# Kernel tuning notes

Measured on AMD Instinct MI355X. Metric: run time of the kernel, lower is better.

The kernel has to match this reference:

```python
import jax, jax.numpy as jnp
import numpy as np

B, S, DIM = 2, 2048, 4096
H, KV = 32, 8
HD = DIM // H          # 128
REP = H // KV          # 4


def _rope_tables(seq_len, head_dim, base=10000.0):
    inv_freq = 1.0 / (base ** (jnp.arange(0, head_dim, 2, dtype=jnp.float32) / head_dim))
    t = jnp.arange(seq_len, dtype=jnp.float32)
    freqs = jnp.outer(t, inv_freq)                      # [S, D/2]
    emb = jnp.concatenate([freqs, freqs], axis=-1)      # [S, D]
    return jnp.cos(emb)[:, None, :], jnp.sin(emb)[:, None, :]  # [S,1,D]


def setup_inputs() -> dict:
    key = jax.random.key(0)
    kx, kq, kk, kv, ko = jax.random.split(key, 5)
    x = jax.random.normal(kx, (B, S, DIM), dtype=jnp.float32)
    cos, sin = _rope_tables(S, HD)
    s = 0.02
    Wq = jax.random.normal(kq, (DIM, H * HD), dtype=jnp.float32) * s
    Wk = jax.random.normal(kk, (DIM, KV * HD), dtype=jnp.float32) * s
    Wv = jax.random.normal(kv, (DIM, KV * HD), dtype=jnp.float32) * s
    Wo = jax.random.normal(ko, (H * HD, DIM), dtype=jnp.float32) * s
    return {"x": x, "cos": cos, "sin": sin, "Wq": Wq, "Wk": Wk, "Wv": Wv, "Wo": Wo}


def _rotate_half(t):
    t1, t2 = jnp.split(t, 2, axis=-1)
    return jnp.concatenate([-t2, t1], axis=-1)


def reference(x, cos, sin, Wq, Wk, Wv, Wo):
    b, s, _ = x.shape
    q = (x @ Wq).reshape(b, s, H, HD)
    k = (x @ Wk).reshape(b, s, KV, HD)
    v = (x @ Wv).reshape(b, s, KV, HD)
    # RoPE (cos/sin broadcast [S,1,D] -> [B,S,H,D])
    q = q * cos + _rotate_half(q) * sin
    k = k * cos + _rotate_half(k) * sin
    # grouped-head attention: avoid materializing repeated K/V
    q = q.reshape(b, s, KV, REP, HD)
    scale = 1.0 / jnp.sqrt(jnp.asarray(HD, dtype=x.dtype))
    scores = jnp.einsum('bqgrd,bkgd->bgrqk', q, k) * scale  # [B,KV,REP,S,S]
    causal = jnp.tril(jnp.ones((s, s), dtype=bool))
    scores = jnp.where(causal, scores, jnp.finfo(scores.dtype).min)
    attn = jax.nn.softmax(scores, axis=-1)
    out = jnp.einsum('bgrqk,bkgd->bqgrd', attn, v)          # [B,S,KV,REP,HD]
    out = out.reshape(b, s, H * HD)
    return out @ Wo
```

## Files before the change

### kernel.cpp

```cpp
#include <hip/hip_runtime.h>
#include <hip/hip_bf16.h>

#define B_   2
#define S_   2048
#define DIM_ 4096
#define H_   32
#define KV_  8
#define HD_  128
#define MROWS_ (B_ * S_)
#define KVD_ (KV_ * HD_)
#define QKVN_ (DIM_ + 2 * KVD_)

typedef __attribute__((ext_vector_type(8))) short short8;
typedef __attribute__((ext_vector_type(4))) float floatx4;

__device__ __forceinline__ unsigned int f2bf(float f) {
    union { float f; unsigned int u; } v; v.f = f;
    unsigned int lsb = (v.u >> 16) & 1u;
    v.u += 0x7fffu + lsb;
    return v.u >> 16;
}
__device__ __forceinline__ unsigned int pack2bf(float lo, float hi) {
    return f2bf(lo) | (f2bf(hi) << 16);
}

__device__ __forceinline__ uint4 load8cvt(const float* __restrict__ src) {
    const float4 a = ((const float4*)src)[0];
    const float4 b = ((const float4*)src)[1];
    uint4 r;
    r.x = pack2bf(a.x, a.y);
    r.y = pack2bf(a.z, a.w);
    r.z = pack2bf(b.x, b.y);
    r.w = pack2bf(b.z, b.w);
    return r;
}

__device__ __forceinline__ void storeC(float* p, float v) { *p = v; }
__device__ __forceinline__ void storeC(__hip_bfloat16* p, float v) { *p = __float2bfloat16(v); }

__device__ __forceinline__ void gload16(const unsigned short* g, unsigned short* l)
{
    __builtin_amdgcn_global_load_lds(
        (const __attribute__((address_space(1))) void*)g,
        (__attribute__((address_space(3))) void*)l,
        16, 0, 0);
}

__global__ __launch_bounds__(256)
void convert_bf16(const float* __restrict__ X, unsigned short* __restrict__ Y, int total8)
{
    const int i = blockIdx.x * 256 + threadIdx.x;
    if (i >= total8) return;
    uint4 v = load8cvt(X + (size_t)i * 8);
    *(uint4*)(Y + (size_t)i * 8) = v;
}

__global__ __launch_bounds__(256)
void wtrans(const float* __restrict__ W, unsigned short* __restrict__ Wt, int K, int N)
{
    __shared__ float tile[64][65];
    const int n0 = blockIdx.x * 64;
    const int k0 = blockIdx.y * 64;
    const int t  = threadIdx.x;
    #pragma unroll
    for (int it = 0; it < 4; ++it) {
        const int seg = t + it * 256;
        const int r   = seg >> 4;
        const int c   = (seg & 15) << 2;
        const float4 v = *(const float4*)&W[(size_t)(k0 + r) * N + n0 + c];
        tile[r][c]     = v.x;
        tile[r][c + 1] = v.y;
        tile[r][c + 2] = v.z;
        tile[r][c + 3] = v.w;
    }
    __syncthreads();
    const int n  = t >> 2;
    const int ks = (t & 3) << 4;
    unsigned int ob[8];
    #pragma unroll
    for (int j = 0; j < 8; ++j)
        ob[j] = pack2bf(tile[ks + 2 * j][n], tile[ks + 2 * j + 1][n]);
    uint4* dst = (uint4*)&Wt[(size_t)(n0 + n) * K + k0 + ks];
    dst[0] = ((const uint4*)ob)[0];
    dst[1] = ((const uint4*)ob)[1];
}

template <typename TC>
__global__ __launch_bounds__(256)
void gemm_bt(const unsigned short* __restrict__ A,
             const unsigned short* __restrict__ Bt,
             TC* __restrict__ C,
             int M, int N, int K)
{
    __shared__ unsigned short As[128 * 32];
    __shared__ unsigned short Bs[128 * 32];

    const int tid  = threadIdx.x;
    const int lane = tid & 63;
    const int w    = tid >> 6;
    const int wm   = (w >> 1) * 64;
    const int wn   = (w & 1) * 64;

    const int gx  = gridDim.x;
    const int nwg = gx * gridDim.y;
    int lid = blockIdx.y * gx + blockIdx.x;
    if ((nwg & 7) == 0) {
        const int q = nwg >> 3;
        lid = (lid & 7) * q + (lid >> 3);
    }
    const int m0 = (lid / gx) * 128;
    const int n0 = (lid % gx) * 128;

    const int fm   = lane & 15;
    const int fk   = (lane >> 4) * 8;

    floatx4 acc[4][4] = {};

    const int sr = tid >> 2;
    const int sk = (tid & 3) * 8;
    const unsigned short* ga0 = A  + (size_t)(m0 + sr) * K + sk;
    const unsigned short* ga1 = ga0 + (size_t)64 * K;
    const unsigned short* gb0 = Bt + (size_t)(n0 + sr) * K + sk;
    const unsigned short* gb1 = gb0 + (size_t)64 * K;
    unsigned short* lA = As + w * 512;
    unsigned short* lB = Bs + w * 512;

    for (int k0 = 0; k0 < K; k0 += 32) {
        gload16(ga0 + k0, lA);
        gload16(ga1 + k0, lA + 2048);
        gload16(gb0 + k0, lB);
        gload16(gb1 + k0, lB + 2048);
        __syncthreads();

        short8 af[4], bf[4];
        #pragma unroll
        for (int i = 0; i < 4; ++i) {
            af[i] = *(const short8*)&As[(wm + i * 16 + fm) * 32 + fk];
            bf[i] = *(const short8*)&Bs[(wn + i * 16 + fm) * 32 + fk];
        }
        #pragma unroll
        for (int mi = 0; mi < 4; ++mi)
            #pragma unroll
            for (int ni = 0; ni < 4; ++ni)
                acc[mi][ni] = __builtin_amdgcn_mfma_f32_16x16x32_bf16(
                    af[mi], bf[ni], acc[mi][ni], 0, 0, 0);
        __syncthreads();
    }

    const int cl = lane & 15;
    const int rq = (lane >> 4) * 4;
    #pragma unroll
    for (int mi = 0; mi < 4; ++mi) {
        #pragma unroll
        for (int ni = 0; ni < 4; ++ni) {
            const int col = n0 + wn + ni * 16 + cl;
            #pragma unroll
            for (int r = 0; r < 4; ++r) {
                const int row = m0 + wm + mi * 16 + rq + r;
                storeC(C + (size_t)row * N + col, acc[mi][ni][r]);
            }
        }
    }
}

__global__ void rope_kernel(unsigned short* __restrict__ T,
                            const float* __restrict__ cosb,
                            const float* __restrict__ sinb,
                            int NH, int coloff, int total)
{
    int idx = blockIdx.x * blockDim.x + threadIdx.x;
    if (idx >= total) return;
    const int dh   = idx & 63;
    const int rest = idx >> 6;
    const int h    = rest % NH;
    const int bs   = rest / NH;
    const int s    = bs & (S_ - 1);
    const size_t base = (size_t)bs * QKVN_ + coloff + h * HD_;
    const float t1 = __bfloat162float(*(__hip_bfloat16*)&T[base + dh]);
    const float t2 = __bfloat162float(*(__hip_bfloat16*)&T[base + dh + 64]);
    const float c1 = cosb[s * HD_ + dh];
    const float s1 = sinb[s * HD_ + dh];
    const float c2 = cosb[s * HD_ + dh + 64];
    const float s2 = sinb[s * HD_ + dh + 64];
    T[base + dh]      = (unsigned short)f2bf(t1 * c1 - t2 * s1);
    T[base + dh + 64] = (unsigned short)f2bf(t2 * c2 + t1 * s2);
}

__global__ __launch_bounds__(256)
void attn_mfma(const unsigned short* __restrict__ QKV,
               __hip_bfloat16* __restrict__ O)
{
    const int bx = blockIdx.x;
    const int bh = blockIdx.y;
    const int b  = bh >> 5;
    const int h  = bh & 31;
    const int g  = h >> 2;

    __shared__ unsigned short lds[27136];
    unsigned short* KsF = lds;
    unsigned short* VtF = lds + 8704;
    unsigned short* PsF = lds + 17920;
    unsigned short* Es  = lds;

    const int tid  = threadIdx.x;
    const int lane = tid & 63;
    const int w    = tid >> 6;
    const int fm   = lane & 15;
    const int quad = lane >> 4;
    const int fk   = quad * 8;

    const float scale = 0.08838834764831845f;
    short8 ones;
    #pragma unroll
    for (int j = 0; j < 8; ++j) ones[j] = (short)0x3F80;

    const int key  = tid >> 2;
    const int d0   = (tid & 3) * 32;
    const int vcol = key ^ ((tid & 3) << 4);
    const unsigned short* Kp = QKV + DIM_ + g * HD_;
    const unsigned short* Vp = QKV + DIM_ + KVD_ + g * HD_;
    const size_t gbase = (size_t)(b * S_ + key) * QKVN_ + d0;
    const size_t gstep = (size_t)64 * QKVN_;
    uint4 kreg[4], vreg[4];

    for (int pass = 0; pass < 2; ++pass) {
        const int qt = pass ? bx : (15 - bx);
        const int q0 = qt * 128;
        const int qrow_base = q0 + w * 32;

        short8 qf[2][4];
        #pragma unroll
        for (int mt = 0; mt < 2; ++mt) {
            const int row = qrow_base + mt * 16 + fm;
            const unsigned short* qp = QKV + (size_t)(b * S_ + row) * QKVN_ + h * HD_;
            #pragma unroll
            for (int dt = 0; dt < 4; ++dt)
                qf[mt][dt] = *(const short8*)(qp + dt * 32 + fk);
        }

        floatx4 o_acc[2][8] = {};
        floatx4 sum_acc[2] = {};
        float m_r[2][4];
        #pragma unroll
        for (int mt = 0; mt < 2; ++mt)
            #pragma unroll
            for (int r = 0; r < 4; ++r) m_r[mt][r] = -1e30f;

        const int ktiles = 2 * (qt + 1);
        {
            const uint4* kp = (const uint4*)(Kp + gbase);
            const uint4* vp = (const uint4*)(Vp + gbase);
            #pragma unroll
            for (int i = 0; i < 4; ++i) { kreg[i] = kp[i]; vreg[i] = vp[i]; }
        }

        for (int kt = 0; kt < ktiles; ++kt) {
            const int k0 = kt * 64;
            __syncthreads();
            {
                *(uint4*)&KsF[key * 136 + d0]      = kreg[0];
                *(uint4*)&KsF[key * 136 + d0 + 8]  = kreg[1];
                *(uint4*)&KsF[key * 136 + d0 + 16] = kreg[2];
                *(uint4*)&KsF[key * 136 + d0 + 24] = kreg[3];
                const unsigned short* vs = (const unsigned short*)vreg;
                #pragma unroll
                for (int i = 0; i < 32; ++i)
                    VtF[(d0 + i) * 72 + vcol] = vs[i];
            }
            __syncthreads();
            if (kt + 1 < ktiles) {
                const uint4* kp = (const uint4*)(Kp + gbase + (size_t)(kt + 1) * gstep);
                const uint4* vp = (const uint4*)(Vp + gbase + (size_t)(kt + 1) * gstep);
                #pragma unroll
                for (int i = 0; i < 4; ++i) { kreg[i] = kp[i]; vreg[i] = vp[i]; }
            }

            if (k0 > qrow_base + 31) continue;

            floatx4 s_acc[2][4] = {};
            #pragma unroll
            for (int dt = 0; dt < 4; ++dt) {
                #pragma unroll
                for (int nt = 0; nt < 4; ++nt) {
                    short8 bfr = *(const short8*)&KsF[(nt * 16 + fm) * 136 + dt * 32 + fk];
                    #pragma unroll
                    for (int mt = 0; mt < 2; ++mt)
                        s_acc[mt][nt] = __builtin_amdgcn_mfma_f32_16x16x32_bf16(
                            qf[mt][dt], bfr, s_acc[mt][nt], 0, 0, 0);
                }
            }

            const bool needmask = (k0 + 63 > qrow_base);
            #pragma unroll
            for (int mt = 0; mt < 2; ++mt) {
                const int rowq0 = qrow_base + mt * 16 + quad * 4;
                #pragma unroll
                for (int r = 0; r < 4; ++r) {
                    if (needmask) {
                        const int rowq = rowq0 + r;
                        #pragma unroll
                        for (int nt = 0; nt < 4; ++nt) {
                            const int c = k0 + nt * 16 + fm;
                            if (c > rowq) s_acc[mt][nt][r] = -1e30f;
                        }
                    }
                    float mx = fmaxf(fmaxf(s_acc[mt][0][r], s_acc[mt][1][r]),
                                     fmaxf(s_acc[mt][2][r], s_acc[mt][3][r]));
                    #pragma unroll
                    for (int off = 1; off < 16; off <<= 1)
                        mx = fmaxf(mx, __shfl_xor(mx, off));
                    float mcur = m_r[mt][r];
                    if (__any(mx > mcur + 90.5f)) {
                        const float mnew = fmaxf(mcur, mx);
                        const float alpha = __expf((mcur - mnew) * scale);
                        #pragma unroll
                        for (int nt = 0; nt < 8; ++nt)
                            o_acc[mt][nt][r] *= alpha;
                        sum_acc[mt][r] *= alpha;
                        m_r[mt][r] = mnew;
                        mcur = mnew;
                    }
                    const int prow = mt * 16 + quad * 4 + r;
                    #pragma unroll
                    for (int nt = 0; nt < 4; ++nt) {
                        const float p = __expf((s_acc[mt][nt][r] - mcur) * scale);
                        PsF[(w * 32 + prow) * 72 + ((nt * 16 + fm) ^ (quad << 3))] =
                            (unsigned short)f2bf(p);
                    }
                }
            }

            #pragma unroll
            for (int ct = 0; ct < 2; ++ct) {
                short8 af[2];
                #pragma unroll
                for (int mt = 0; mt < 2; ++mt)
                    af[mt] = *(const short8*)
                        &PsF[(w * 32 + mt * 16 + fm) * 72 + ct * 32 + ((quad ^ (fm >> 2)) << 3)];
                #pragma unroll
                for (int mt = 0; mt < 2; ++mt)
                    sum_acc[mt] = __builtin_amdgcn_mfma_f32_16x16x32_bf16(
                        af[mt], ones, sum_acc[mt], 0, 0, 0);
                #pragma unroll
                for (int nt = 0; nt < 8; ++nt) {
                    short8 bfr = *(const short8*)
                        &VtF[(nt * 16 + fm) * 72 + ((ct * 32 + fk) ^ ((nt >> 1) << 4))];
                    #pragma unroll
                    for (int mt = 0; mt < 2; ++mt)
                        o_acc[mt][nt] = __builtin_amdgcn_mfma_f32_16x16x32_bf16(
                            af[mt], bfr, o_acc[mt][nt], 0, 0, 0);
                }
            }
        }

        __syncthreads();
        unsigned short* Ew = Es + w * (32 * 136);
        #pragma unroll
        for (int mt = 0; mt < 2; ++mt) {
            #pragma unroll
            for (int r = 0; r < 4; ++r) {
                const float inv_l = 1.f / sum_acc[mt][r];
                const int prow = mt * 16 + quad * 4 + r;
                #pragma unroll
                for (int nt = 0; nt < 8; ++nt)
                    Ew[prow * 136 + nt * 16 + fm] =
                        (unsigned short)f2bf(o_acc[mt][nt][r] * inv_l);
            }
        }
        __syncthreads();
        #pragma unroll
        for (int mt = 0; mt < 2; ++mt) {
            const int rowE = mt * 16 + fm;
            const unsigned short* src = Ew + rowE * 136 + quad * 32;
            __hip_bfloat16* op = O + ((size_t)(b * S_ + qrow_base + rowE) * H_ + h) * HD_
                                   + quad * 32;
            uint4 v0 = *(const uint4*)(src);
            uint4 v1 = *(const uint4*)(src + 8);
            uint4 v2 = *(const uint4*)(src + 16);
            uint4 v3 = *(const uint4*)(src + 24);
            *(uint4*)(op)      = v0;
            *(uint4*)(op + 8)  = v1;
            *(uint4*)(op + 16) = v2;
            *(uint4*)(op + 24) = v3;
        }
    }
}

extern "C" void kernel_launch(void* const* d_in, const int* in_sizes, int n_in,
                              void* d_out, int out_size, void* d_ws, size_t ws_size,
                              hipStream_t stream)
{
    const float* x    = (const float*)d_in[0];
    const float* cosb = (const float*)d_in[1];
    const float* sinb = (const float*)d_in[2];
    const float* Wq   = (const float*)d_in[3];
    const float* Wk   = (const float*)d_in[4];
    const float* Wv   = (const float*)d_in[5];
    const float* Wo   = (const float*)d_in[6];
    float* out = (float*)d_out;

    char* ws = (char*)d_ws;
    const size_t MB = 1024 * 1024;
    unsigned short* Xb  = (unsigned short*)(ws);
    unsigned short* Ab  = (unsigned short*)(ws);
    unsigned short* WT  = (unsigned short*)(ws + 32 * MB);
    unsigned short* WoT = (unsigned short*)(ws + 32 * MB);
    unsigned short* QKV = (unsigned short*)(ws + 80 * MB);

    unsigned short* WTq = WT;
    unsigned short* WTk = WT + (size_t)DIM_ * DIM_;
    unsigned short* WTv = WT + (size_t)(DIM_ + KVD_) * DIM_;

    dim3 blk(256);

    convert_bf16<<<dim3((MROWS_ * DIM_) / 8 / 256), blk, 0, stream>>>(
        x, Xb, (MROWS_ * DIM_) / 8);

    wtrans<<<dim3(DIM_ / 64, DIM_ / 64), blk, 0, stream>>>(Wq, WTq, DIM_, DIM_);
    wtrans<<<dim3(KVD_ / 64, DIM_ / 64), blk, 0, stream>>>(Wk, WTk, DIM_, KVD_);
    wtrans<<<dim3(KVD_ / 64, DIM_ / 64), blk, 0, stream>>>(Wv, WTv, DIM_, KVD_);

    gemm_bt<__hip_bfloat16><<<dim3(QKVN_ / 128, MROWS_ / 128), blk, 0, stream>>>(
        Xb, WT, (__hip_bfloat16*)QKV, MROWS_, QKVN_, DIM_);

    wtrans<<<dim3(DIM_ / 64, DIM_ / 64), blk, 0, stream>>>(Wo, WoT, DIM_, DIM_);

    {
        int totq = MROWS_ * H_ * 64;
        int totk = MROWS_ * KV_ * 64;
        rope_kernel<<<(totq + 255) / 256, blk, 0, stream>>>(
            QKV, cosb, sinb, H_, 0, totq);
        rope_kernel<<<(totk + 255) / 256, blk, 0, stream>>>(
            QKV, cosb, sinb, KV_, DIM_, totk);
    }

    attn_mfma<<<dim3(8, B_ * H_), blk, 0, stream>>>(
        QKV, (__hip_bfloat16*)Ab);

    gemm_bt<float><<<dim3(DIM_ / 128, MROWS_ / 128), blk, 0, stream>>>(
        Ab, WoT, out, MROWS_, DIM_, DIM_);
}
```

Measured before the change: 1.101 ms.

## Replace GEMM with 256x256-tile double-buffered swizzled LDS kernel

Rewrites the bf16 GEMM used for the QKV and output projections to use 256x256 output tiles with 512 threads, a K-step of 64, and double-buffered shared memory filled by async global loads with explicit vmcnt waits. LDS columns are XOR-swizzled to avoid bank conflicts, and MFMA sections run at raised wave priority. The larger tiles raise arithmetic intensity and the overlap hides global-load latency. In exchange the kernel uses 128KB of LDS and more accumulator registers per thread, and the grid becomes small (e.g. 256 blocks for the output GEMM), which may leave CUs underused.

```diff
diff --git a/kernel.cpp b/kernel.cpp
--- a/kernel.cpp
+++ b/kernel.cpp
@@ -86,20 +86,22 @@
 }
 
 template <typename TC>
-__global__ __launch_bounds__(256)
-void gemm_bt(const unsigned short* __restrict__ A,
+__global__ __launch_bounds__(512)
+void gemm256(const unsigned short* __restrict__ A,
              const unsigned short* __restrict__ Bt,
              TC* __restrict__ C,
              int M, int N, int K)
 {
-    __shared__ unsigned short As[128 * 32];
-    __shared__ unsigned short Bs[128 * 32];
+    __shared__ unsigned short As[2][16384];
+    __shared__ unsigned short Bs[2][16384];
 
     const int tid  = threadIdx.x;
     const int lane = tid & 63;
     const int w    = tid >> 6;
-    const int wm   = (w >> 1) * 64;
-    const int wn   = (w & 1) * 64;
+    const int wm   = (w >> 2) * 128;
+    const int wn   = (w & 3) * 64;
+    const int fm   = lane & 15;
+    const int quad = lane >> 4;
 
     const int gx  = gridDim.x;
     const int nwg = gx * gridDim.y;
@@ -108,49 +110,68 @@
         const int q = nwg >> 3;
         lid = (lid & 7) * q + (lid >> 3);
     }
-    const int m0 = (lid / gx) * 128;
-    const int n0 = (lid % gx) * 128;
-
-    const int fm   = lane & 15;
-    const int fk   = (lane >> 4) * 8;
-
-    floatx4 acc[4][4] = {};
-
-    const int sr = tid >> 2;
-    const int sk = (tid & 3) * 8;
-    const unsigned short* ga0 = A  + (size_t)(m0 + sr) * K + sk;
-    const unsigned short* ga1 = ga0 + (size_t)64 * K;
-    const unsigned short* gb0 = Bt + (size_t)(n0 + sr) * K + sk;
-    const unsigned short* gb1 = gb0 + (size_t)64 * K;
-    unsigned short* lA = As + w * 512;
-    unsigned short* lB = Bs + w * 512;
-
-    for (int k0 = 0; k0 < K; k0 += 32) {
-        gload16(ga0 + k0, lA);
-        gload16(ga1 + k0, lA + 2048);
-        gload16(gb0 + k0, lB);
-        gload16(gb1 + k0, lB + 2048);
-        __syncthreads();
-
-        short8 af[4], bf[4];
-        #pragma unroll
-        for (int i = 0; i < 4; ++i) {
-            af[i] = *(const short8*)&As[(wm + i * 16 + fm) * 32 + fk];
-            bf[i] = *(const short8*)&Bs[(wn + i * 16 + fm) * 32 + fk];
-        }
-        #pragma unroll
-        for (int mi = 0; mi < 4; ++mi)
+    const int m0 = (lid / gx) * 256;
+    const int n0 = (lid % gx) * 256;
+
+    floatx4 acc[8][4] = {};
+
+    const int rowb = tid >> 3;
+    const int koff = ((tid & 7) ^ ((tid >> 5) & 3)) * 8;
+    const unsigned short* gA = A  + (size_t)(m0 + rowb) * K + koff;
+    const unsigned short* gB = Bt + (size_t)(n0 + rowb) * K + koff;
+    const int NT = K >> 6;
+
+#define STAGE256(kt, sel) do {                                                \
+    const size_t ko_ = (size_t)(kt) * 64;                                     \
+    _Pragma("unroll")                                                         \
+    for (int i_ = 0; i_ < 4; ++i_)                                            \
+        gload16(gA + (size_t)(i_ * 64) * K + ko_, &As[sel][i_ * 4096 + w * 512]); \
+    _Pragma("unroll")                                                         \
+    for (int i_ = 0; i_ < 4; ++i_)                                            \
+        gload16(gB + (size_t)(i_ * 64) * K + ko_, &Bs[sel][i_ * 4096 + w * 512]); \
+} while (0)
+
+    STAGE256(0, 0);
+    STAGE256(1, 1);
+
+    for (int kt = 0; kt < NT; ++kt) {
+        if (kt + 1 < NT) { asm volatile("s_waitcnt vmcnt(8)" ::: "memory"); }
+        else             { asm volatile("s_waitcnt vmcnt(0)" ::: "memory"); }
+        __builtin_amdgcn_s_barrier();
+        __builtin_amdgcn_sched_barrier(0);
+
+        const unsigned short* bufA = As[kt & 1];
+        const unsigned short* bufB = Bs[kt & 1];
+        #pragma unroll
+        for (int win = 0; win < 2; ++win) {
+            const int pc = ((win * 4 + quad) ^ (fm >> 2)) * 8;
+            short8 afr[8], bfr[4];
+            #pragma unroll
+            for (int mi = 0; mi < 8; ++mi)
+                afr[mi] = *(const short8*)&bufA[(wm + mi * 16 + fm) * 64 + pc];
             #pragma unroll
             for (int ni = 0; ni < 4; ++ni)
-                acc[mi][ni] = __builtin_amdgcn_mfma_f32_16x16x32_bf16(
-                    af[mi], bf[ni], acc[mi][ni], 0, 0, 0);
-        __syncthreads();
-    }
-
-    const int cl = lane & 15;
-    const int rq = (lane >> 4) * 4;
+                bfr[ni] = *(const short8*)&bufB[(wn + ni * 16 + fm) * 64 + pc];
+            __builtin_amdgcn_s_setprio(1);
+            #pragma unroll
+            for (int mi = 0; mi < 8; ++mi)
+                #pragma unroll
+                for (int ni = 0; ni < 4; ++ni)
+                    acc[mi][ni] = __builtin_amdgcn_mfma_f32_16x16x32_bf16(
+                        afr[mi], bfr[ni], acc[mi][ni], 0, 0, 0);
+            __builtin_amdgcn_s_setprio(0);
+        }
+        asm volatile("s_waitcnt lgkmcnt(0)" ::: "memory");
+        __builtin_amdgcn_s_barrier();
+        __builtin_amdgcn_sched_barrier(0);
+        if (kt + 2 < NT) STAGE256(kt + 2, kt & 1);
+    }
+#undef STAGE256
+
+    const int cl = fm;
+    const int rq = quad * 4;
     #pragma unroll
-    for (int mi = 0; mi < 4; ++mi) {
+    for (int mi = 0; mi < 8; ++mi) {
         #pragma unroll
         for (int ni = 0; ni < 4; ++ni) {
             const int col = n0 + wn + ni * 16 + cl;
@@ -412,6 +433,7 @@
     unsigned short* WTv = WT + (size_t)(DIM_ + KVD_) * DIM_;
 
     dim3 blk(256);
+    dim3 blk512(512);
 
     convert_bf16<<<dim3((MROWS_ * DIM_) / 8 / 256), blk, 0, stream>>>(
         x, Xb, (MROWS_ * DIM_) / 8);
@@ -420,7 +442,7 @@
     wtrans<<<dim3(KVD_ / 64, DIM_ / 64), blk, 0, stream>>>(Wk, WTk, DIM_, KVD_);
     wtrans<<<dim3(KVD_ / 64, DIM_ / 64), blk, 0, stream>>>(Wv, WTv, DIM_, KVD_);
 
-    gemm_bt<__hip_bfloat16><<<dim3(QKVN_ / 128, MROWS_ / 128), blk, 0, stream>>>(
+    gemm256<__hip_bfloat16><<<dim3(QKVN_ / 256, MROWS_ / 256), blk512, 0, stream>>>(
         Xb, WT, (__hip_bfloat16*)QKV, MROWS_, QKVN_, DIM_);
 
     wtrans<<<dim3(DIM_ / 64, DIM_ / 64), blk, 0, stream>>>(Wo, WoT, DIM_, DIM_);
@@ -437,6 +459,6 @@
     attn_mfma<<<dim3(8, B_ * H_), blk, 0, stream>>>(
         QKV, (__hip_bfloat16*)Ab);
 
-    gemm_bt<float><<<dim3(DIM_ / 128, MROWS_ / 128), blk, 0, stream>>>(
+    gemm256<float><<<dim3(DIM_ / 256, MROWS_ / 256), blk512, 0, stream>>>(
         Ab, WoT, out, MROWS_, DIM_, DIM_);
 }
```

Result: no change. 1.081 ms (-1.8%).
